# Kernel optimization log

Measured on AMD Instinct MI355X. Metric: run time of the kernel, lower is better.

Reference implementation:

```python
import jax, jax.numpy as jnp
import numpy as np

N = 50000        # nodes
E = 1600000      # edges (before self loops)
IN_DIM = 300     # input feature size
HID = 256        # hidden size
HEADS = 8
OC = HID // HEADS  # out channels per head = 32
LAYERS = 4
B = 1024         # number of target pairs
C = 3            # num classes
NEG_SLOPE = 0.2  # PyG GATConv leaky_relu slope


def setup_inputs() -> dict:
    key = jax.random.key(0)
    ks = jax.random.split(key, 12)

    def glorot(k, shape):
        lim = np.sqrt(6.0 / (shape[-2] + shape[-1]))
        return jax.random.uniform(k, shape, jnp.float32, -lim, lim)

    return {
        "x": jax.random.normal(ks[0], (N, IN_DIM), jnp.float32),
        "edge_index": jax.random.randint(ks[1], (2, E), 0, N, jnp.int64 if jax.config.jax_enable_x64 else jnp.int32),
        "target_mask": jax.random.randint(ks[2], (B, 2), 0, N, jnp.int64 if jax.config.jax_enable_x64 else jnp.int32),
        # lin1: [IN_DIM, HID] (stored pre-transposed vs torch)
        "lin1_W": glorot(ks[3], (IN_DIM, HID)),
        "lin1_b": jnp.zeros((HID,), jnp.float32),
        # stacked GATConv params
        "convs_W": glorot(ks[4], (LAYERS, HID, HEADS * OC)),
        "convs_att_dst": glorot(ks[5], (LAYERS, HEADS, OC)),  # att half applied to x_i (target)
        "convs_att_src": glorot(ks[6], (LAYERS, HEADS, OC)),  # att half applied to x_j (source)
        "convs_b": jnp.zeros((LAYERS, HID), jnp.float32),
        # lin3: [2*HID, C]
        "lin3_W": glorot(ks[7], (2 * HID, C)),
        "lin3_b": jnp.zeros((C,), jnp.float32),
    }


def gat_layer(h, src, tgt, W, att_dst, att_src, bias):
    """PyG-style GATConv (concat heads), edge list already includes self loops.
    h: [N, HID]; src/tgt: [E+N]; W: [HID, HEADS*OC]."""
    hw = (h @ W).reshape(N, HEADS, OC)
    # per-node attention scores, gathered per-edge (avoids materializing concat features)
    s_dst = jnp.einsum("nho,ho->nh", hw, att_dst)  # score for target role
    s_src = jnp.einsum("nho,ho->nh", hw, att_src)  # score for source role
    alpha = jax.nn.leaky_relu(s_dst[tgt] + s_src[src], NEG_SLOPE)  # [Etot, HEADS]
    # softmax over edges sharing the same target node (self loops => no empty segments)
    m = jax.ops.segment_max(alpha, tgt, num_segments=N)
    ex = jnp.exp(alpha - m[tgt])
    denom = jax.ops.segment_sum(ex, tgt, num_segments=N)
    a = ex / (denom[tgt] + 1e-16)
    # weighted scatter-aggregate of source features
    out = jax.ops.segment_sum(hw[src] * a[:, :, None], tgt, num_segments=N)  # [N, HEADS, OC]
    return out.reshape(N, HEADS * OC) + bias


def reference(x, edge_index, target_mask, lin1_W, lin1_b, convs_W,
              convs_att_dst, convs_att_src, convs_b, lin3_W, lin3_b):
    # add self loops once (PyG GATConv does this per layer; same edge set every layer)
    loop = jnp.arange(N, dtype=edge_index.dtype)
    src = jnp.concatenate([edge_index[0], loop])
    tgt = jnp.concatenate([edge_index[1], loop])

    h = x @ lin1_W + lin1_b
    for l in range(LAYERS):
        h = jax.nn.elu(gat_layer(h, src, tgt, convs_W[l],
                                 convs_att_dst[l], convs_att_src[l], convs_b[l]))
    # gather the two target nodes per sample and flatten -> [B, 2*HID]
    feats = h[target_mask].reshape(B, 2 * HID)
    logits = feats @ lin3_W + lin3_b
    return logits
```

## Files before the change

### kernel.cpp

```cpp
#include <hip/hip_runtime.h>
#include <math.h>

#define N_NODES 50000
#define N_PAD   50048
#define E_EDGES 1600000
#define ETOT    (E_EDGES + N_NODES)
#define EPAD    (E_EDGES + 8 * N_NODES)
#define IN_DIM  300
#define KP1     320
#define HID     256
#define HEADS   8
#define OC      32
#define LAYERS  4
#define BSAMP   1024
#define NEG_SLOPE 0.2f
#define DEG_CAP 128

#define NB     8
#define NPB    6250
#define BCAP   262144
#define NBLK_P 512
#define NBLK_S 196
#define NBLK_B 2048

typedef unsigned long long ull;
typedef _Float16 half8 __attribute__((ext_vector_type(8)));
typedef _Float16 half4v __attribute__((ext_vector_type(4)));
typedef float f32x4 __attribute__((ext_vector_type(4)));

#define GLDS16(g, l) __builtin_amdgcn_global_load_lds( \
    (const __attribute__((address_space(1))) void*)(g), \
    (__attribute__((address_space(3))) void*)(l), 16, 0, 0)


__global__ __launch_bounds__(256) void part_count_kernel(const int* __restrict__ tgt,
                                                         int* __restrict__ gcount) {
    __shared__ int cnt[NB];
    if (threadIdx.x < NB) cnt[threadIdx.x] = 0;
    __syncthreads();
    const int chunk = (ETOT + NBLK_P - 1) / NBLK_P;
    int beg = blockIdx.x * chunk;
    int end = min(beg + chunk, ETOT);
    for (int e = beg + threadIdx.x; e < end; e += 256) {
        int t_ = (e < E_EDGES) ? tgt[e] : (e - E_EDGES);
        atomicAdd(&cnt[t_ / NPB], 1);
    }
    __syncthreads();
    if (threadIdx.x < NB) gcount[blockIdx.x * NB + threadIdx.x] = cnt[threadIdx.x];
}

__global__ __launch_bounds__(512) void part_scan_kernel(const int* __restrict__ gcount,
                                                        int* __restrict__ goff,
                                                        int* __restrict__ bcnt) {
    __shared__ int arr[NBLK_P][NB];
    int k = threadIdx.x;
    int4 a = ((const int4*)gcount)[k * 2];
    int4 b = ((const int4*)gcount)[k * 2 + 1];
    int own[NB] = {a.x, a.y, a.z, a.w, b.x, b.y, b.z, b.w};
    #pragma unroll
    for (int j = 0; j < NB; j++) arr[k][j] = own[j];
    __syncthreads();
    for (int off = 1; off < NBLK_P; off <<= 1) {
        int tmp[NB];
        #pragma unroll
        for (int j = 0; j < NB; j++) tmp[j] = (k >= off) ? arr[k - off][j] : 0;
        __syncthreads();
        #pragma unroll
        for (int j = 0; j < NB; j++) arr[k][j] += tmp[j];
        __syncthreads();
    }
    int ex[NB];
    #pragma unroll
    for (int j = 0; j < NB; j++) ex[j] = arr[k][j] - own[j];
    ((int4*)goff)[k * 2]     = make_int4(ex[0], ex[1], ex[2], ex[3]);
    ((int4*)goff)[k * 2 + 1] = make_int4(ex[4], ex[5], ex[6], ex[7]);
    if (k == NBLK_P - 1) {
        #pragma unroll
        for (int j = 0; j < NB; j++) bcnt[j] = arr[k][j];
    }
}

__global__ __launch_bounds__(256) void part_scatter_kernel(const int* __restrict__ src,
                                                           const int* __restrict__ tgt,
                                                           const int* __restrict__ goff,
                                                           ull* __restrict__ bpart) {
    __shared__ int cur[NB];
    if (threadIdx.x < NB) cur[threadIdx.x] = goff[blockIdx.x * NB + threadIdx.x];
    __syncthreads();
    const int chunk = (ETOT + NBLK_P - 1) / NBLK_P;
    int beg = blockIdx.x * chunk;
    int end = min(beg + chunk, ETOT);
    for (int e = beg + threadIdx.x; e < end; e += 256) {
        int s_, t_;
        if (e < E_EDGES) { s_ = src[e]; t_ = tgt[e]; }
        else             { s_ = t_ = e - E_EDGES; }
        int b = t_ / NPB;
        int pos = atomicAdd(&cur[b], 1);
        bpart[(size_t)b * BCAP + pos] = ((ull)(unsigned)t_ << 32) | (unsigned)s_;
    }
}

__global__ __launch_bounds__(256) void count_edges_kernel(const ull* __restrict__ bpart,
                                                          const int* __restrict__ bcnt,
                                                          int* counts) {
    int b = blockIdx.x & (NB - 1);
    int ib = blockIdx.x >> 3;
    int nblk = gridDim.x >> 3;
    int nb = bcnt[b];
    const ull* bp = bpart + (size_t)b * BCAP;
    for (int i = ib * 256 + threadIdx.x; i < nb; i += nblk * 256)
        atomicAdd(&counts[(int)(bp[i] >> 32)], 1);
}

__global__ __launch_bounds__(256) void scan1_kernel(const int* __restrict__ counts,
                                                    int* __restrict__ row_ptr,
                                                    int* __restrict__ bsum) {
    __shared__ int sums[256];
    int t = threadIdx.x;
    int i = blockIdx.x * 256 + t;
    int c = (i < N_NODES) ? ((counts[i] + 7) & ~7) : 0;
    sums[t] = c;
    __syncthreads();
    for (int off = 1; off < 256; off <<= 1) {
        int a = sums[t];
        int u = (t >= off) ? sums[t - off] : 0;
        __syncthreads();
        sums[t] = a + u;
        __syncthreads();
    }
    if (i < N_NODES) row_ptr[i] = sums[t] - c;
    if (t == 255) bsum[blockIdx.x] = sums[255];
}

__global__ __launch_bounds__(256) void scan2_kernel(const int* __restrict__ bsum,
                                                    int* __restrict__ boff,
                                                    int* __restrict__ row_ptr) {
    __shared__ int sums[256];
    int t = threadIdx.x;
    int b = (t < NBLK_S) ? bsum[t] : 0;
    sums[t] = b;
    __syncthreads();
    for (int off = 1; off < 256; off <<= 1) {
        int a = sums[t];
        int u = (t >= off) ? sums[t - off] : 0;
        __syncthreads();
        sums[t] = a + u;
        __syncthreads();
    }
    if (t < NBLK_S) boff[t] = sums[t] - b;
    if (t == 255) row_ptr[N_NODES] = sums[255];
}

__global__ __launch_bounds__(256) void scan3_kernel(int* __restrict__ row_ptr,
                                                    const int* __restrict__ boff,
                                                    int* __restrict__ cursor) {
    int i = blockIdx.x * 256 + threadIdx.x;
    if (i >= N_NODES) return;
    int v = row_ptr[i] + boff[blockIdx.x];
    row_ptr[i] = v;
    cursor[i]  = v;
}

__global__ __launch_bounds__(256) void fill_edges_kernel(const ull* __restrict__ bpart,
                                                         const int* __restrict__ bcnt,
                                                         int* cursor, int* __restrict__ col) {
    int b = blockIdx.x & (NB - 1);
    int ib = blockIdx.x >> 3;
    int nblk = gridDim.x >> 3;
    int nb = bcnt[b];
    const ull* bp = bpart + (size_t)b * BCAP;
    for (int i = ib * 256 + threadIdx.x; i < nb; i += nblk * 256) {
        ull pk = bp[i];
        int t_ = (int)(pk >> 32);
        int s_ = (int)pk;
        int pos = atomicAdd(&cursor[t_], 1);
        col[pos] = s_;
    }
}

__global__ __launch_bounds__(256) void pad_edges_kernel(const int* __restrict__ cursor,
                                                        const int* __restrict__ row_ptr,
                                                        int* __restrict__ col) {
    int i = blockIdx.x * 256 + threadIdx.x;
    if (i >= N_NODES) return;
    int e = cursor[i];
    int pe = row_ptr[i + 1];
    for (; e < pe; e++) col[e] = i;
}


__global__ __launch_bounds__(256) void cast_x_kernel(const float* __restrict__ x, _Float16* __restrict__ xh) {
    int i = blockIdx.x * 256 + threadIdx.x;
    if (i >= N_NODES * (KP1 / 8)) return;
    int r = i / (KP1 / 8), c8 = i % (KP1 / 8);
    half8 o;
    const float4* xr = (const float4*)(x + (size_t)r * IN_DIM);
    if (c8 < 37) {
        float4 u = xr[c8 * 2], v = xr[c8 * 2 + 1];
        o[0] = (_Float16)u.x; o[1] = (_Float16)u.y; o[2] = (_Float16)u.z; o[3] = (_Float16)u.w;
        o[4] = (_Float16)v.x; o[5] = (_Float16)v.y; o[6] = (_Float16)v.z; o[7] = (_Float16)v.w;
    } else if (c8 == 37) {
        float4 u = xr[74];
        o[0] = (_Float16)u.x; o[1] = (_Float16)u.y; o[2] = (_Float16)u.z; o[3] = (_Float16)u.w;
        o[4] = o[5] = o[6] = o[7] = (_Float16)0.f;
    } else {
        #pragma unroll
        for (int j = 0; j < 8; j++) o[j] = (_Float16)0.f;
    }
    ((half8*)xh)[i] = o;
}

__global__ __launch_bounds__(256) void cast_w1_kernel(const float* __restrict__ W, _Float16* __restrict__ Wt) {
    int i = blockIdx.x * 256 + threadIdx.x;
    if (i >= HID * KP1) return;
    int n = i / KP1, k = i % KP1;
    float v = (k < IN_DIM) ? W[(size_t)k * HID + n] : 0.f;
    Wt[i] = (_Float16)v;
}

__global__ __launch_bounds__(256) void cast_wc_kernel(const float* __restrict__ W, _Float16* __restrict__ Wt) {
    int i = blockIdx.x * 256 + threadIdx.x;
    if (i >= LAYERS * HID * HID) return;
    int l = i / (HID * HID);
    int r = i % (HID * HID);
    int n = r / HID, k = r % HID;
    Wt[i] = (_Float16)W[(size_t)l * HID * HID + (size_t)k * HID + n];
}

__global__ __launch_bounds__(256) void gemm_mfma_kernel(const _Float16* __restrict__ A,
                                                        const _Float16* __restrict__ Wt,
                                                        const float* __restrict__ bias,
                                                        _Float16* __restrict__ C,
                                                        int M, int Kp, int addbias) {
    __shared__ _Float16 As[128][32];
    __shared__ _Float16 Bs[128][32];
    const int tid = threadIdx.x;
    const int m0 = blockIdx.x * 128;
    const int n0 = blockIdx.y * 128;
    const int w = tid >> 6, lane = tid & 63;
    const int wm = (w & 1) * 64, wn = (w >> 1) * 64;
    const int quad = lane >> 4, m16 = lane & 15;

    f32x4 acc[4][4];
    #pragma unroll
    for (int i = 0; i < 4; i++)
        #pragma unroll
        for (int j = 0; j < 4; j++)
            acc[i][j] = (f32x4){0.f, 0.f, 0.f, 0.f};

    char* lA = (char*)&As[0][0] + w * 1024;
    char* lB = (char*)&Bs[0][0] + w * 1024;

    for (int k0 = 0; k0 < Kp; k0 += 32) {
        #pragma unroll
        for (int i = 0; i < 2; i++) {
            int seg = tid + i * 256;
            int row = seg >> 2, off = seg & 3;
            GLDS16(&A[(size_t)(m0 + row) * Kp + k0 + off * 8], lA + i * 4096);
            GLDS16(&Wt[(size_t)(n0 + row) * Kp + k0 + off * 8], lB + i * 4096);
        }
        __syncthreads();

        half8 af[4], bf[4];
        #pragma unroll
        for (int i = 0; i < 4; i++) {
            af[i] = *(const half8*)&As[wm + i * 16 + m16][quad * 8];
            bf[i] = *(const half8*)&Bs[wn + i * 16 + m16][quad * 8];
        }
        #pragma unroll
        for (int mi = 0; mi < 4; mi++)
            #pragma unroll
            for (int ni = 0; ni < 4; ni++)
                acc[mi][ni] = __builtin_amdgcn_mfma_f32_16x16x32_f16(af[mi], bf[ni], acc[mi][ni], 0, 0, 0);
        __syncthreads();
    }

    #pragma unroll
    for (int mi = 0; mi < 4; mi++) {
        #pragma unroll
        for (int r = 0; r < 4; r++) {
            int row = m0 + wm + mi * 16 + quad * 4 + r;
            if (row < M) {
                #pragma unroll
                for (int ni = 0; ni < 4; ni++) {
                    int colg = n0 + wn + ni * 16 + m16;
                    float v = acc[mi][ni][r];
                    if (addbias) v += bias[colg];
                    C[(size_t)row * HID + colg] = (_Float16)v;
                }
            }
        }
    }
}

__global__ __launch_bounds__(256) void score_kernel(const _Float16* __restrict__ hw,
                                                    const float* __restrict__ att_dst,
                                                    const float* __restrict__ att_src,
                                                    float* __restrict__ s_dst,
                                                    float* __restrict__ s_src) {
    int wv = threadIdx.x >> 6, lane = threadIdx.x & 63;
    int nd = lane >> 3, hd = lane & 7;
    float4 ad[8], as4[8];
    const float4* A4d = (const float4*)att_dst;
    const float4* A4s = (const float4*)att_src;
    #pragma unroll
    for (int j = 0; j < 8; j++) { ad[j] = A4d[hd * 8 + j]; as4[j] = A4s[hd * 8 + j]; }
    const half8* hw8 = (const half8*)hw;
    int nwaves = gridDim.x * 4;
    for (int g = blockIdx.x * 4 + wv; g < N_NODES / 8; g += nwaves) {
        int node = g * 8 + nd;
        float sd = 0.f, ss = 0.f;
        #pragma unroll
        for (int k = 0; k < 4; k++) {
            half8 v = hw8[(size_t)node * 32 + hd * 4 + k];
            #pragma unroll
            for (int i = 0; i < 8; i++) {
                float f = (float)v[i];
                int q = k * 8 + i;
                sd += f * ((const float*)&ad[q >> 2])[q & 3];
                ss += f * ((const float*)&as4[q >> 2])[q & 3];
            }
        }
        s_dst[(size_t)g * 64 + lane] = sd;
        s_src[(size_t)g * 64 + lane] = ss;
    }
}

__global__ __launch_bounds__(256) void agg_kernel(const int* __restrict__ row_ptr,
                                                  const int* __restrict__ deg_arr,
                                                  const int* __restrict__ col,
                                                  const float* __restrict__ s_dst,
                                                  const float* __restrict__ s_src,
                                                  const _Float16* __restrict__ hw,
                                                  const float* __restrict__ bias,
                                                  _Float16* __restrict__ h_out) {
    __shared__ float exL[4][DEG_CAP * 8];
    __shared__ int  snL[4][DEG_CAP];

    int wv   = threadIdx.x >> 6;
    int lane = threadIdx.x & 63;
    int t = blockIdx.x * 4 + wv;
    if (t >= N_NODES) return;

    int start = row_ptr[t];
    int pdeg  = row_ptr[t + 1] - start;
    int deg   = deg_arr[t];

    int eh  = lane & 7;
    int ech = lane >> 3;
    float sd = s_dst[(size_t)t * HEADS + eh];

    if (pdeg <= DEG_CAP) {
        int ngrp = pdeg >> 3;
        float dsum = 0.f;
        for (int g = 0; g < ngrp; g++) {
            int slot = g * 8 + ech;
            int sn = col[start + slot];
            float a = sd + s_src[(size_t)sn * HEADS + eh];
            a = (a > 0.f) ? a : NEG_SLOPE * a;
            float exv = (slot < deg) ? __expf(a) : 0.f;
            exL[wv][slot * 8 + eh] = exv;
            if (eh == 0) snL[wv][slot] = sn;
            dsum += exv;
        }
        dsum += __shfl_xor(dsum, 8);
        dsum += __shfl_xor(dsum, 16);
        dsum += __shfl_xor(dsum, 32);

        int p  = lane >> 5;
        int c  = lane & 31;
        int hh = c >> 2;
        float inv = 1.f / (__shfl(dsum, hh) + 1e-16f);

        const half8* hw8 = (const half8*)hw;
        float acc[8] = {0.f, 0.f, 0.f, 0.f, 0.f, 0.f, 0.f, 0.f};

        for (int g = 0; g < ngrp; g++) {
            int base = g * 8;
            int   sns[4];
            half8 v[4];
            float ex[4];
            #pragma unroll
            for (int j = 0; j < 4; j++) sns[j] = snL[wv][base + 2 * j + p];
            #pragma unroll
            for (int j = 0; j < 4; j++) v[j] = hw8[(size_t)sns[j] * 32 + c];
            #pragma unroll
            for (int j = 0; j < 4; j++) ex[j] = exL[wv][(base + 2 * j + p) * 8 + hh];
            #pragma unroll
            for (int j = 0; j < 4; j++)
                #pragma unroll
                for (int i = 0; i < 8; i++)
                    acc[i] += ex[j] * (float)v[j][i];
        }

        #pragma unroll
        for (int i = 0; i < 8; i++) acc[i] += __shfl_xor(acc[i], 32);

        if (p == 0) {
            half8 ov;
            #pragma unroll
            for (int i = 0; i < 8; i++) {
                float o = acc[i] * inv + bias[c * 8 + i];
                o = (o > 0.f) ? o : (__expf(o) - 1.f);
                ov[i] = (_Float16)o;
            }
            ((half8*)h_out)[(size_t)t * 32 + c] = ov;
        }
    } else {
        int end = start + deg;
        float mx = -1e30f;
        for (int base = start; base < end; base += 8) {
            int e = base + ech;
            if (e < end) {
                int sn = col[e];
                float a = sd + s_src[(size_t)sn * HEADS + eh];
                a = (a > 0.f) ? a : NEG_SLOPE * a;
                mx = fmaxf(mx, a);
            }
        }
        mx = fmaxf(mx, __shfl_xor(mx, 8));
        mx = fmaxf(mx, __shfl_xor(mx, 16));
        mx = fmaxf(mx, __shfl_xor(mx, 32));

        float4 acc = {0.f, 0.f, 0.f, 0.f};
        float dsum = 0.f;
        const half4v* hw4 = (const half4v*)hw;
        int chead = lane >> 3;
        for (int base = start; base < end; base += 8) {
            int e = base + ech;
            float exv = 0.f;
            int sn = 0;
            if (e < end) {
                sn = col[e];
                float a = sd + s_src[(size_t)sn * HEADS + eh];
                a = (a > 0.f) ? a : NEG_SLOPE * a;
                exv = __expf(a - mx);
                dsum += exv;
            }
            int cnt = min(8, end - base);
            for (int j = 0; j < cnt; j++) {
                float exj = __shfl(exv, j * 8 + chead);
                int  snj  = __shfl(sn,  j * 8);
                half4v v = hw4[(size_t)snj * 64 + lane];
                acc.x += exj * (float)v[0];
                acc.y += exj * (float)v[1];
                acc.z += exj * (float)v[2];
                acc.w += exj * (float)v[3];
            }
        }
        dsum += __shfl_xor(dsum, 8);
        dsum += __shfl_xor(dsum, 16);
        dsum += __shfl_xor(dsum, 32);
        float den = __shfl(dsum, chead) + 1e-16f;
        float inv = 1.f / den;
        int cb = lane * 4;
        float o[4] = {acc.x * inv + bias[cb + 0], acc.y * inv + bias[cb + 1],
                      acc.z * inv + bias[cb + 2], acc.w * inv + bias[cb + 3]};
        #pragma unroll
        for (int i = 0; i < 4; i++) o[i] = (o[i] > 0.f) ? o[i] : (__expf(o[i]) - 1.f);
        half4v ov;
        ov[0] = (_Float16)o[0]; ov[1] = (_Float16)o[1];
        ov[2] = (_Float16)o[2]; ov[3] = (_Float16)o[3];
        ((half4v*)h_out)[(size_t)t * 64 + lane] = ov;
    }
}

__global__ __launch_bounds__(256) void head_kernel(const _Float16* __restrict__ h,
                                                   const int* __restrict__ target_mask,
                                                   const float* __restrict__ W,
                                                   const float* __restrict__ b,
                                                   float* __restrict__ out) {
    int s = blockIdx.x;
    int t = threadIdx.x;
    int n0 = target_mask[s * 2 + 0];
    int n1 = target_mask[s * 2 + 1];
    float f0 = (float)h[(size_t)n0 * HID + t];
    float f1 = (float)h[(size_t)n1 * HID + t];
    float a0 = f0 * W[t * 3 + 0] + f1 * W[(t + 256) * 3 + 0];
    float a1 = f0 * W[t * 3 + 1] + f1 * W[(t + 256) * 3 + 1];
    float a2 = f0 * W[t * 3 + 2] + f1 * W[(t + 256) * 3 + 2];
    #pragma unroll
    for (int off = 32; off >= 1; off >>= 1) {
        a0 += __shfl_xor(a0, off);
        a1 += __shfl_xor(a1, off);
        a2 += __shfl_xor(a2, off);
    }
    __shared__ float red[4][3];
    int wv = t >> 6, ln = t & 63;
    if (ln == 0) { red[wv][0] = a0; red[wv][1] = a1; red[wv][2] = a2; }
    __syncthreads();
    if (t < 3) {
        out[s * 3 + t] = red[0][t] + red[1][t] + red[2][t] + red[3][t] + b[t];
    }
}


extern "C" void kernel_launch(void* const* d_in, const int* in_sizes, int n_in,
                              void* d_out, int out_size, void* d_ws, size_t ws_size,
                              hipStream_t stream) {
    const float* x        = (const float*)d_in[0];
    const int*   eidx     = (const int*)  d_in[1];
    const int*   tmask    = (const int*)  d_in[2];
    const float* lin1_W   = (const float*)d_in[3];
    const float* lin1_b   = (const float*)d_in[4];
    const float* convs_W  = (const float*)d_in[5];
    const float* att_dst  = (const float*)d_in[6];
    const float* att_src  = (const float*)d_in[7];
    const float* convs_b  = (const float*)d_in[8];
    const float* lin3_W   = (const float*)d_in[9];
    const float* lin3_b   = (const float*)d_in[10];
    float* out = (float*)d_out;

    char* ws = (char*)d_ws;
    size_t off = 0;
    auto alloc = [&](size_t bytes) -> void* {
        void* p = ws + off;
        off = (off + bytes + 255) & ~(size_t)255;
        return p;
    };
    _Float16* xh   = (_Float16*)alloc((size_t)N_PAD * KP1 * 2);
    _Float16* h    = (_Float16*)alloc((size_t)N_PAD * HID * 2);
    _Float16* hw   = (_Float16*)alloc((size_t)N_NODES * HID * 2);
    _Float16* w1t  = (_Float16*)alloc((size_t)HID * KP1 * 2);
    _Float16* wct  = (_Float16*)alloc((size_t)LAYERS * HID * HID * 2);
    float* sdst    = (float*)alloc((size_t)N_NODES * HEADS * 4);
    float* ssrc    = (float*)alloc((size_t)N_NODES * HEADS * 4);
    int*   counts  = (int*)  alloc((size_t)N_NODES * 4);
    int*   rowptr  = (int*)  alloc((size_t)(N_NODES + 1) * 4);
    int*   cursor  = (int*)  alloc((size_t)N_NODES * 4);
    int*   col     = (int*)  alloc((size_t)EPAD * 4);
    ull*   bpart   = (ull*)  alloc((size_t)NB * BCAP * 8);
    int*   bcnt    = (int*)  alloc((size_t)NB * 4);
    int*   gcount  = (int*)  alloc((size_t)NBLK_P * NB * 4);
    int*   goff    = (int*)  alloc((size_t)NBLK_P * NB * 4);
    int*   bsum    = (int*)  alloc((size_t)NBLK_S * 4);
    int*   boff    = (int*)  alloc((size_t)NBLK_S * 4);

    const int* src = eidx;
    const int* tgt = eidx + E_EDGES;

    hipMemsetAsync(counts, 0, (size_t)N_NODES * 4, stream);
    part_count_kernel<<<NBLK_P, 256, 0, stream>>>(tgt, gcount);
    part_scan_kernel<<<1, NBLK_P, 0, stream>>>(gcount, goff, bcnt);
    part_scatter_kernel<<<NBLK_P, 256, 0, stream>>>(src, tgt, goff, bpart);
    count_edges_kernel<<<NBLK_B, 256, 0, stream>>>(bpart, bcnt, counts);
    scan1_kernel<<<NBLK_S, 256, 0, stream>>>(counts, rowptr, bsum);
    scan2_kernel<<<1, 256, 0, stream>>>(bsum, boff, rowptr);
    scan3_kernel<<<NBLK_S, 256, 0, stream>>>(rowptr, boff, cursor);
    fill_edges_kernel<<<NBLK_B, 256, 0, stream>>>(bpart, bcnt, cursor, col);
    pad_edges_kernel<<<(N_NODES + 255) / 256, 256, 0, stream>>>(cursor, rowptr, col);

    cast_x_kernel<<<(N_NODES * (KP1 / 8) + 255) / 256, 256, 0, stream>>>(x, xh);
    cast_w1_kernel<<<(HID * KP1 + 255) / 256, 256, 0, stream>>>(lin1_W, w1t);
    cast_wc_kernel<<<(LAYERS * HID * HID + 255) / 256, 256, 0, stream>>>(convs_W, wct);

    gemm_mfma_kernel<<<dim3((N_NODES + 127) / 128, HID / 128), 256, 0, stream>>>(
        xh, w1t, lin1_b, h, N_NODES, KP1, 1);

    for (int l = 0; l < LAYERS; l++) {
        gemm_mfma_kernel<<<dim3((N_NODES + 127) / 128, HID / 128), 256, 0, stream>>>(
            h, wct + (size_t)l * HID * HID, nullptr, hw, N_NODES, HID, 0);
        score_kernel<<<256, 256, 0, stream>>>(
            hw, att_dst + (size_t)l * HEADS * OC, att_src + (size_t)l * HEADS * OC, sdst, ssrc);
        agg_kernel<<<(N_NODES + 3) / 4, 256, 0, stream>>>(
            rowptr, counts, col, sdst, ssrc, hw, convs_b + (size_t)l * HID, h);
    }

    head_kernel<<<BSAMP, 256, 0, stream>>>(h, tmask, lin3_W, lin3_b, out);
}
```

Measured before the change: 941.1 us.

## Partition edges by target and source block so CSR columns are source-sorted

Edges are now partitioned into 64 buckets keyed by (target block, source block) rather than 8 target buckets. Per-node per-source-block counts and cursors place each node's neighbor list grouped by source block. The aim is better cache locality when the aggregation kernel gathers source features, and spreading the fill-time atomics over more counters. In exchange the CSR build has more kernels and a larger counts/cursor buffer, and each bucket is capped at 32768 edges, which is tight for the expected ~26k per bucket.

```diff
diff --git a/kernel.cpp b/kernel.cpp
--- a/kernel.cpp
+++ b/kernel.cpp
@@ -17,8 +17,9 @@
 #define DEG_CAP 128
 
 #define NB     8
+#define NSB    64
 #define NPB    6250
-#define BCAP   262144
+#define BCAP2  32768
 #define NBLK_P 512
 #define NBLK_S 196
 #define NBLK_B 2048
@@ -33,59 +34,11 @@
     (__attribute__((address_space(3))) void*)(l), 16, 0, 0)
 
 
-__global__ __launch_bounds__(256) void part_count_kernel(const int* __restrict__ tgt,
+__global__ __launch_bounds__(256) void part_count_kernel(const int* __restrict__ src,
+                                                         const int* __restrict__ tgt,
                                                          int* __restrict__ gcount) {
-    __shared__ int cnt[NB];
-    if (threadIdx.x < NB) cnt[threadIdx.x] = 0;
-    __syncthreads();
-    const int chunk = (ETOT + NBLK_P - 1) / NBLK_P;
-    int beg = blockIdx.x * chunk;
-    int end = min(beg + chunk, ETOT);
-    for (int e = beg + threadIdx.x; e < end; e += 256) {
-        int t_ = (e < E_EDGES) ? tgt[e] : (e - E_EDGES);
-        atomicAdd(&cnt[t_ / NPB], 1);
-    }
-    __syncthreads();
-    if (threadIdx.x < NB) gcount[blockIdx.x * NB + threadIdx.x] = cnt[threadIdx.x];
-}
-
-__global__ __launch_bounds__(512) void part_scan_kernel(const int* __restrict__ gcount,
-                                                        int* __restrict__ goff,
-                                                        int* __restrict__ bcnt) {
-    __shared__ int arr[NBLK_P][NB];
-    int k = threadIdx.x;
-    int4 a = ((const int4*)gcount)[k * 2];
-    int4 b = ((const int4*)gcount)[k * 2 + 1];
-    int own[NB] = {a.x, a.y, a.z, a.w, b.x, b.y, b.z, b.w};
-    #pragma unroll
-    for (int j = 0; j < NB; j++) arr[k][j] = own[j];
-    __syncthreads();
-    for (int off = 1; off < NBLK_P; off <<= 1) {
-        int tmp[NB];
-        #pragma unroll
-        for (int j = 0; j < NB; j++) tmp[j] = (k >= off) ? arr[k - off][j] : 0;
-        __syncthreads();
-        #pragma unroll
-        for (int j = 0; j < NB; j++) arr[k][j] += tmp[j];
-        __syncthreads();
-    }
-    int ex[NB];
-    #pragma unroll
-    for (int j = 0; j < NB; j++) ex[j] = arr[k][j] - own[j];
-    ((int4*)goff)[k * 2]     = make_int4(ex[0], ex[1], ex[2], ex[3]);
-    ((int4*)goff)[k * 2 + 1] = make_int4(ex[4], ex[5], ex[6], ex[7]);
-    if (k == NBLK_P - 1) {
-        #pragma unroll
-        for (int j = 0; j < NB; j++) bcnt[j] = arr[k][j];
-    }
-}
-
-__global__ __launch_bounds__(256) void part_scatter_kernel(const int* __restrict__ src,
-                                                           const int* __restrict__ tgt,
-                                                           const int* __restrict__ goff,
-                                                           ull* __restrict__ bpart) {
-    __shared__ int cur[NB];
-    if (threadIdx.x < NB) cur[threadIdx.x] = goff[blockIdx.x * NB + threadIdx.x];
+    __shared__ int cnt[NSB];
+    if (threadIdx.x < NSB) cnt[threadIdx.x] = 0;
     __syncthreads();
     const int chunk = (ETOT + NBLK_P - 1) / NBLK_P;
     int beg = blockIdx.x * chunk;
@@ -94,22 +47,79 @@
         int s_, t_;
         if (e < E_EDGES) { s_ = src[e]; t_ = tgt[e]; }
         else             { s_ = t_ = e - E_EDGES; }
-        int b = t_ / NPB;
+        atomicAdd(&cnt[(t_ / NPB) * NB + (s_ / NPB)], 1);
+    }
+    __syncthreads();
+    if (threadIdx.x < NSB) gcount[blockIdx.x * NSB + threadIdx.x] = cnt[threadIdx.x];
+}
+
+__global__ __launch_bounds__(256) void part_scan_kernel(const int* __restrict__ gcount,
+                                                        int* __restrict__ goff,
+                                                        int* __restrict__ bcnt) {
+    __shared__ int sums[256];
+    int b = blockIdx.x;
+    int t = threadIdx.x;
+    int g0 = gcount[(2 * t) * NSB + b];
+    int g1 = gcount[(2 * t + 1) * NSB + b];
+    int s = g0 + g1;
+    sums[t] = s;
+    __syncthreads();
+    for (int off = 1; off < 256; off <<= 1) {
+        int a = sums[t];
+        int u = (t >= off) ? sums[t - off] : 0;
+        __syncthreads();
+        sums[t] = a + u;
+        __syncthreads();
+    }
+    int ex = sums[t] - s;
+    goff[(2 * t) * NSB + b]     = ex;
+    goff[(2 * t + 1) * NSB + b] = ex + g0;
+    if (t == 255) bcnt[b] = sums[255];
+}
+
+__global__ __launch_bounds__(256) void part_scatter_kernel(const int* __restrict__ src,
+                                                           const int* __restrict__ tgt,
+                                                           const int* __restrict__ goff,
+                                                           ull* __restrict__ bpart) {
+    __shared__ int cur[NSB];
+    if (threadIdx.x < NSB) cur[threadIdx.x] = goff[blockIdx.x * NSB + threadIdx.x];
+    __syncthreads();
+    const int chunk = (ETOT + NBLK_P - 1) / NBLK_P;
+    int beg = blockIdx.x * chunk;
+    int end = min(beg + chunk, ETOT);
+    for (int e = beg + threadIdx.x; e < end; e += 256) {
+        int s_, t_;
+        if (e < E_EDGES) { s_ = src[e]; t_ = tgt[e]; }
+        else             { s_ = t_ = e - E_EDGES; }
+        int b = (t_ / NPB) * NB + (s_ / NPB);
         int pos = atomicAdd(&cur[b], 1);
-        bpart[(size_t)b * BCAP + pos] = ((ull)(unsigned)t_ << 32) | (unsigned)s_;
-    }
-}
-
-__global__ __launch_bounds__(256) void count_edges_kernel(const ull* __restrict__ bpart,
-                                                          const int* __restrict__ bcnt,
-                                                          int* counts) {
-    int b = blockIdx.x & (NB - 1);
+        bpart[(size_t)b * BCAP2 + pos] = ((ull)(unsigned)t_ << 32) | (unsigned)s_;
+    }
+}
+
+__global__ __launch_bounds__(256) void count_sub_kernel(const ull* __restrict__ bpart,
+                                                        const int* __restrict__ bcnt,
+                                                        int* counts2) {
+    int tb = blockIdx.x & (NB - 1);
     int ib = blockIdx.x >> 3;
     int nblk = gridDim.x >> 3;
-    int nb = bcnt[b];
-    const ull* bp = bpart + (size_t)b * BCAP;
-    for (int i = ib * 256 + threadIdx.x; i < nb; i += nblk * 256)
-        atomicAdd(&counts[(int)(bp[i] >> 32)], 1);
+    #pragma unroll
+    for (int sb = 0; sb < NB; sb++) {
+        int p = tb * NB + sb;
+        int nb = bcnt[p];
+        const ull* bp = bpart + (size_t)p * BCAP2;
+        for (int i = ib * 256 + threadIdx.x; i < nb; i += nblk * 256)
+            atomicAdd(&counts2[(size_t)(int)(bp[i] >> 32) * NB + sb], 1);
+    }
+}
+
+__global__ __launch_bounds__(256) void deg_kernel(const int* __restrict__ counts2,
+                                                  int* __restrict__ counts) {
+    int i = blockIdx.x * 256 + threadIdx.x;
+    if (i >= N_NODES) return;
+    int4 a = ((const int4*)counts2)[i * 2];
+    int4 b = ((const int4*)counts2)[i * 2 + 1];
+    counts[i] = a.x + a.y + a.z + a.w + b.x + b.y + b.z + b.w;
 }
 
 __global__ __launch_bounds__(256) void scan1_kernel(const int* __restrict__ counts,
@@ -153,37 +163,55 @@
 
 __global__ __launch_bounds__(256) void scan3_kernel(int* __restrict__ row_ptr,
                                                     const int* __restrict__ boff,
-                                                    int* __restrict__ cursor) {
+                                                    const int* __restrict__ counts2,
+                                                    int* __restrict__ cursor2) {
     int i = blockIdx.x * 256 + threadIdx.x;
     if (i >= N_NODES) return;
     int v = row_ptr[i] + boff[blockIdx.x];
     row_ptr[i] = v;
-    cursor[i]  = v;
+    int4 a = ((const int4*)counts2)[i * 2];
+    int4 b = ((const int4*)counts2)[i * 2 + 1];
+    int c[NB] = {a.x, a.y, a.z, a.w, b.x, b.y, b.z, b.w};
+    int run = v;
+    int4 o0, o1;
+    o0.x = run; run += c[0];
+    o0.y = run; run += c[1];
+    o0.z = run; run += c[2];
+    o0.w = run; run += c[3];
+    o1.x = run; run += c[4];
+    o1.y = run; run += c[5];
+    o1.z = run; run += c[6];
+    o1.w = run;
+    ((int4*)cursor2)[i * 2]     = o0;
+    ((int4*)cursor2)[i * 2 + 1] = o1;
 }
 
 __global__ __launch_bounds__(256) void fill_edges_kernel(const ull* __restrict__ bpart,
                                                          const int* __restrict__ bcnt,
-                                                         int* cursor, int* __restrict__ col) {
-    int b = blockIdx.x & (NB - 1);
+                                                         int* cursor2, int* __restrict__ col) {
+    int tb = blockIdx.x & (NB - 1);
     int ib = blockIdx.x >> 3;
     int nblk = gridDim.x >> 3;
-    int nb = bcnt[b];
-    const ull* bp = bpart + (size_t)b * BCAP;
-    for (int i = ib * 256 + threadIdx.x; i < nb; i += nblk * 256) {
-        ull pk = bp[i];
-        int t_ = (int)(pk >> 32);
-        int s_ = (int)pk;
-        int pos = atomicAdd(&cursor[t_], 1);
-        col[pos] = s_;
-    }
-}
-
-__global__ __launch_bounds__(256) void pad_edges_kernel(const int* __restrict__ cursor,
+    #pragma unroll
+    for (int sb = 0; sb < NB; sb++) {
+        int p = tb * NB + sb;
+        int nb = bcnt[p];
+        const ull* bp = bpart + (size_t)p * BCAP2;
+        for (int i = ib * 256 + threadIdx.x; i < nb; i += nblk * 256) {
+            ull pk = bp[i];
+            int t_ = (int)(pk >> 32);
+            int pos = atomicAdd(&cursor2[(size_t)t_ * NB + sb], 1);
+            col[pos] = (int)pk;
+        }
+    }
+}
+
+__global__ __launch_bounds__(256) void pad_edges_kernel(const int* __restrict__ counts,
                                                         const int* __restrict__ row_ptr,
                                                         int* __restrict__ col) {
     int i = blockIdx.x * 256 + threadIdx.x;
     if (i >= N_NODES) return;
-    int e = cursor[i];
+    int e = row_ptr[i] + counts[i];
     int pe = row_ptr[i + 1];
     for (; e < pe; e++) col[e] = i;
 }
@@ -526,29 +554,31 @@
     float* sdst    = (float*)alloc((size_t)N_NODES * HEADS * 4);
     float* ssrc    = (float*)alloc((size_t)N_NODES * HEADS * 4);
     int*   counts  = (int*)  alloc((size_t)N_NODES * 4);
+    int*   counts2 = (int*)  alloc((size_t)N_NODES * NB * 4);
+    int*   cursor2 = (int*)  alloc((size_t)N_NODES * NB * 4);
     int*   rowptr  = (int*)  alloc((size_t)(N_NODES + 1) * 4);
-    int*   cursor  = (int*)  alloc((size_t)N_NODES * 4);
     int*   col     = (int*)  alloc((size_t)EPAD * 4);
-    ull*   bpart   = (ull*)  alloc((size_t)NB * BCAP * 8);
-    int*   bcnt    = (int*)  alloc((size_t)NB * 4);
-    int*   gcount  = (int*)  alloc((size_t)NBLK_P * NB * 4);
-    int*   goff    = (int*)  alloc((size_t)NBLK_P * NB * 4);
+    ull*   bpart   = (ull*)  alloc((size_t)NSB * BCAP2 * 8);
+    int*   bcnt    = (int*)  alloc((size_t)NSB * 4);
+    int*   gcount  = (int*)  alloc((size_t)NBLK_P * NSB * 4);
+    int*   goff    = (int*)  alloc((size_t)NBLK_P * NSB * 4);
     int*   bsum    = (int*)  alloc((size_t)NBLK_S * 4);
     int*   boff    = (int*)  alloc((size_t)NBLK_S * 4);
 
     const int* src = eidx;
     const int* tgt = eidx + E_EDGES;
 
-    hipMemsetAsync(counts, 0, (size_t)N_NODES * 4, stream);
-    part_count_kernel<<<NBLK_P, 256, 0, stream>>>(tgt, gcount);
-    part_scan_kernel<<<1, NBLK_P, 0, stream>>>(gcount, goff, bcnt);
+    hipMemsetAsync(counts2, 0, (size_t)N_NODES * NB * 4, stream);
+    part_count_kernel<<<NBLK_P, 256, 0, stream>>>(src, tgt, gcount);
+    part_scan_kernel<<<NSB, 256, 0, stream>>>(gcount, goff, bcnt);
     part_scatter_kernel<<<NBLK_P, 256, 0, stream>>>(src, tgt, goff, bpart);
-    count_edges_kernel<<<NBLK_B, 256, 0, stream>>>(bpart, bcnt, counts);
+    count_sub_kernel<<<NBLK_B, 256, 0, stream>>>(bpart, bcnt, counts2);
+    deg_kernel<<<(N_NODES + 255) / 256, 256, 0, stream>>>(counts2, counts);
     scan1_kernel<<<NBLK_S, 256, 0, stream>>>(counts, rowptr, bsum);
     scan2_kernel<<<1, 256, 0, stream>>>(bsum, boff, rowptr);
-    scan3_kernel<<<NBLK_S, 256, 0, stream>>>(rowptr, boff, cursor);
-    fill_edges_kernel<<<NBLK_B, 256, 0, stream>>>(bpart, bcnt, cursor, col);
-    pad_edges_kernel<<<(N_NODES + 255) / 256, 256, 0, stream>>>(cursor, rowptr, col);
+    scan3_kernel<<<NBLK_S, 256, 0, stream>>>(rowptr, boff, counts2, cursor2);
+    fill_edges_kernel<<<NBLK_B, 256, 0, stream>>>(bpart, bcnt, cursor2, col);
+    pad_edges_kernel<<<(N_NODES + 255) / 256, 256, 0, stream>>>(counts, rowptr, col);
 
     cast_x_kernel<<<(N_NODES * (KP1 / 8) + 255) / 256, 256, 0, stream>>>(x, xh);
     cast_w1_kernel<<<(HID * KP1 + 255) / 256, 256, 0, stream>>>(lin1_W, w1t);
```

New measurement: 945.1 us. Within noise of the previous version (+0.4%).
